# Kernel tuning notes

Measured on AMD Instinct MI355X. Metric: run time of the kernel, lower is better.

Reference implementation:

```python
import jax, jax.numpy as jnp
import numpy as np

B, S, IN, E, H, NH = 32, 1024, 16, 128, 256, 4
DH = E // NH
EPS = 1e-5


def _ln(x, g, b):
    mu = jnp.mean(x, axis=-1, keepdims=True)
    var = jnp.mean(jnp.square(x - mu), axis=-1, keepdims=True)
    return (x - mu) * jax.lax.rsqrt(var + EPS) * g + b


def setup_inputs() -> dict:
    key = jax.random.key(0)
    ks = iter(jax.random.split(key, 32))
    n = lambda shape, s=0.02: jax.random.normal(next(ks), shape, jnp.float32) * s
    inp = {
        "x": jax.random.normal(next(ks), (B, S, IN), jnp.float32),
        "mask": jax.random.uniform(next(ks), (B, S), jnp.float32),
        "embed_w": n((E, IN)), "embed_b": jnp.zeros((E,), jnp.float32),
        # 3 encoder layers, params stacked on leading layer axis
        "in_proj_w": n((3, 3 * E, E)), "in_proj_b": jnp.zeros((3, 3 * E), jnp.float32),
        "out_w": n((3, E, E)), "out_b": jnp.zeros((3, E), jnp.float32),
        "ln1_g": jnp.ones((3, E), jnp.float32), "ln1_b": jnp.zeros((3, E), jnp.float32),
        "ln2_g": jnp.ones((3, E), jnp.float32), "ln2_b": jnp.zeros((3, E), jnp.float32),
        "ffn_w1": n((3, E, E)), "ffn_b1": jnp.zeros((3, E), jnp.float32),
        "ffn_w2": n((3, E, E)), "ffn_b2": jnp.zeros((3, E), jnp.float32),
        "cls_w1": n((H, E)), "cls_b1": jnp.zeros((H,), jnp.float32),
        "cls_w2": n((H, H)), "cls_b2": jnp.zeros((H,), jnp.float32),
        "cls_w3": n((H, H)), "cls_b3": jnp.zeros((H,), jnp.float32),
        "cls_w4": n((1, H)), "cls_b4": jnp.zeros((1,), jnp.float32),
    }
    return inp


def _encoder_layer(x, ipw, ipb, ow, ob, g1, b1, g2, b2, w1, fb1, w2, fb2):
    # PyTorch TransformerEncoderLayer, norm_first=False (post-norm), relu FFN
    qkv = x @ ipw.T + ipb                      # [B,S,3E]
    q, k, v = jnp.split(qkv, 3, axis=-1)
    q = q.reshape(B, S, NH, DH).transpose(0, 2, 1, 3)
    k = k.reshape(B, S, NH, DH).transpose(0, 2, 1, 3)
    v = v.reshape(B, S, NH, DH).transpose(0, 2, 1, 3)
    scores = jnp.einsum("bhqd,bhkd->bhqk", q, k) / np.sqrt(DH)  # naive O(S^2) math SDPA
    attn = jax.nn.softmax(scores, axis=-1)
    o = jnp.einsum("bhqk,bhkd->bhqd", attn, v)
    o = o.transpose(0, 2, 1, 3).reshape(B, S, E) @ ow.T + ob
    x = _ln(x + o, g1, b1)
    ff = jax.nn.relu(x @ w1.T + fb1) @ w2.T + fb2
    return _ln(x + ff, g2, b2)


def reference(x, mask, embed_w, embed_b, in_proj_w, in_proj_b, out_w, out_b,
              ln1_g, ln1_b, ln2_g, ln2_b, ffn_w1, ffn_b1, ffn_w2, ffn_b2,
              cls_w1, cls_b1, cls_w2, cls_b2, cls_w3, cls_b3, cls_w4, cls_b4):
    h = jax.nn.relu(x @ embed_w.T + embed_b)   # [B,S,E]
    for i in range(3):
        h = _encoder_layer(h, in_proj_w[i], in_proj_b[i], out_w[i], out_b[i],
                           ln1_g[i], ln1_b[i], ln2_g[i], ln2_b[i],
                           ffn_w1[i], ffn_b1[i], ffn_w2[i], ffn_b2[i])
    pooled = jnp.sum(h * mask[:, :, None], axis=1)  # [B,E] masked sum pool
    z = jax.nn.relu(pooled @ cls_w1.T + cls_b1)
    z = jax.nn.relu(z @ cls_w2.T + cls_b2)
    z = jax.nn.relu(z @ cls_w3.T + cls_b3)
    return jax.nn.sigmoid(z @ cls_w4.T + cls_b4)    # [B,1]
```

## Files before the change

kernel.cpp:

```cpp
#include <hip/hip_runtime.h>
#include <hip/hip_bf16.h>
#include <math.h>

#define B 32
#define S 1024
#define IN_DIM 16
#define E 128
#define NH 4
#define DH 32
#define HDIM 256
#define ROWS (B*S)
#define EPS 1e-5f

#define N_IPW (3*384*128)
#define N_SQ  (3*128*128)
#define NCVT ((N_IPW + 3*N_SQ) / 256)

typedef __bf16 bf16x8 __attribute__((ext_vector_type(8)));
typedef __bf16 bf16x4 __attribute__((ext_vector_type(4)));
typedef __bf16 bf16x2 __attribute__((ext_vector_type(2)));
typedef float f32x4 __attribute__((ext_vector_type(4)));

#define MFMA16 __builtin_amdgcn_mfma_f32_16x16x32_bf16

union BF2U { bf16x2 b; unsigned int u; };
__device__ inline unsigned int pk2(float a, float b) {
    BF2U x; x.b[0] = (__bf16)a; x.b[1] = (__bf16)b; return x.u;
}

union U8 { bf16x8 v8; bf16x4 v4[2]; };
__device__ inline void st8(__bf16* p, bf16x8 v) {
    U8 u; u.v8 = v;
    *(bf16x4*)p = u.v4[0];
    *(bf16x4*)(p + 4) = u.v4[1];
}
__device__ inline bf16x8 ld8(const __bf16* p) {
    U8 u;
    u.v4[0] = *(const bf16x4*)p;
    u.v4[1] = *(const bf16x4*)(p + 4);
    return u.v8;
}

__global__ __launch_bounds__(256) void k_embedcvt(
        const float* __restrict__ ipw, const float* __restrict__ ow,
        const float* __restrict__ w1, const float* __restrict__ w2,
        __bf16* __restrict__ wbo,
        const float* __restrict__ x, const float* __restrict__ W,
        const float* __restrict__ bias, __bf16* __restrict__ hb)
{
    int t = threadIdx.x;
    if (blockIdx.x < NCVT) {
        int i = blockIdx.x * 256 + t;
        float v;
        if (i < N_IPW) v = ipw[i];
        else if (i < N_IPW + N_SQ) v = ow[i - N_IPW];
        else if (i < N_IPW + 2 * N_SQ) v = w1[i - N_IPW - N_SQ];
        else v = w2[i - N_IPW - 2 * N_SQ];
        wbo[i] = (__bf16)v;
        return;
    }
    int row0 = (blockIdx.x - NCVT) * 16;
    __shared__ float xs[16][16];
    xs[t >> 4][t & 15] = x[(row0 + (t >> 4)) * IN_DIM + (t & 15)];
    __syncthreads();
    int sub = t >> 7, tc = t & 127;
    float w[16];
#pragma unroll
    for (int i = 0; i < 16; ++i) w[i] = W[tc * 16 + i];
    float bb = bias[tc];
#pragma unroll
    for (int rr = 0; rr < 8; ++rr) {
        int lr = sub * 8 + rr;
        float acc = bb;
#pragma unroll
        for (int i = 0; i < 16; ++i) acc += xs[lr][i] * w[i];
        hb[(size_t)(row0 + lr) * E + tc] = (__bf16)fmaxf(acc, 0.f);
    }
}

__global__ __launch_bounds__(512, 2) void k_qkvattn(
        const __bf16* __restrict__ hb, const __bf16* __restrict__ Wip,
        const float* __restrict__ bip, __bf16* __restrict__ O)
{
    __shared__ __attribute__((aligned(16))) __bf16 Ksh[1024][36];
    __shared__ __attribute__((aligned(16))) __bf16 Vsh[32][1036];
    __shared__ __attribute__((aligned(16))) __bf16 Pm[8][16][68];

    int t = threadIdx.x, lane = t & 63, wv = t >> 6;
    int l15 = lane & 15, quad = lane >> 4;
    int lb = ((blockIdx.x & 7) << 5) | (blockIdx.x >> 3);
    int half = lb & 1, bh = lb >> 1;
    int hh = bh & 3, b = bh >> 2;

    const __bf16* hpanel = hb + (size_t)b * S * E;

    const float qscale = 0.1767766952966369f * 1.4426950408889634f * 8388608.0f;
    const float C2 = 1065101558.0f;
    const f32x4 cinit = {C2, C2, C2, C2};
    const f32x4 z4 = {0.f, 0.f, 0.f, 0.f};

    bf16x8 bWk[2][4], bWv[2][4];
#pragma unroll
    for (int df = 0; df < 2; ++df)
#pragma unroll
        for (int kc = 0; kc < 4; ++kc) {
            bWk[df][kc] = *(const bf16x8*)&Wip[(size_t)(128 + hh*32 + df*16 + l15)*128 + kc*32 + quad*8];
            bWv[df][kc] = *(const bf16x8*)&Wip[(size_t)(256 + hh*32 + df*16 + l15)*128 + kc*32 + quad*8];
        }
    float bk0 = bip[128 + hh*32 + l15],      bk1 = bip[128 + hh*32 + 16 + l15];
    float bvb0 = bip[256 + hh*32 + l15],     bvb1 = bip[256 + hh*32 + 16 + l15];

    int qrow0 = half*512 + wv*64;
    bf16x8 bQ[4];
    {
        bf16x8 bWq[2][4];
#pragma unroll
        for (int df = 0; df < 2; ++df)
#pragma unroll
            for (int kc = 0; kc < 4; ++kc)
                bWq[df][kc] = *(const bf16x8*)&Wip[(size_t)(hh*32 + df*16 + l15)*128 + kc*32 + quad*8];
        float bq0 = bip[hh*32 + l15], bq1 = bip[hh*32 + 16 + l15];
#pragma unroll
        for (int qf = 0; qf < 4; ++qf) {
            bf16x8 af[4];
#pragma unroll
            for (int kc = 0; kc < 4; ++kc)
                af[kc] = *(const bf16x8*)&hpanel[(size_t)(qrow0 + qf*16 + l15)*128 + kc*32 + quad*8];
            f32x4 a0 = z4, a1 = z4;
#pragma unroll
            for (int kc = 0; kc < 4; ++kc) {
                a0 = MFMA16(af[kc], bWq[0][kc], a0, 0, 0, 0);
                a1 = MFMA16(af[kc], bWq[1][kc], a1, 0, 0, 0);
            }
#pragma unroll
            for (int r = 0; r < 4; ++r) {
                Pm[wv][quad*4 + r][l15]      = (__bf16)((a0[r] + bq0) * qscale);
                Pm[wv][quad*4 + r][16 + l15] = (__bf16)((a1[r] + bq1) * qscale);
            }
            __asm__ __volatile__("" ::: "memory");
            bQ[qf] = ld8(&Pm[wv][l15][quad*8]);
            __asm__ __volatile__("" ::: "memory");
        }
    }

    {
        int srow = wv*16 + l15;
        bf16x8 af[4], ag[4];
#pragma unroll
        for (int kc = 0; kc < 4; ++kc)
            af[kc] = *(const bf16x8*)&hpanel[(size_t)srow*128 + kc*32 + quad*8];
        for (int c = 0; c < 8; ++c) {
            if (c < 7) {
#pragma unroll
                for (int kc = 0; kc < 4; ++kc)
                    ag[kc] = *(const bf16x8*)&hpanel[(size_t)((c+1)*128 + srow)*128 + kc*32 + quad*8];
            }
            f32x4 k0 = z4, k1 = z4, v0 = z4, v1 = z4;
#pragma unroll
            for (int kc = 0; kc < 4; ++kc) {
                k0 = MFMA16(af[kc], bWk[0][kc], k0, 0, 0, 0);
                k1 = MFMA16(af[kc], bWk[1][kc], k1, 0, 0, 0);
                v0 = MFMA16(af[kc], bWv[0][kc], v0, 0, 0, 0);
                v1 = MFMA16(af[kc], bWv[1][kc], v1, 0, 0, 0);
            }
            int s0 = c*128 + wv*16 + quad*4;
#pragma unroll
            for (int r = 0; r < 4; ++r) {
                Ksh[s0 + r][l15]      = (__bf16)(k0[r] + bk0);
                Ksh[s0 + r][16 + l15] = (__bf16)(k1[r] + bk1);
            }
            uint2 u0, u1;
            u0.x = pk2(v0[0] + bvb0, v0[1] + bvb0);
            u0.y = pk2(v0[2] + bvb0, v0[3] + bvb0);
            u1.x = pk2(v1[0] + bvb1, v1[1] + bvb1);
            u1.y = pk2(v1[2] + bvb1, v1[3] + bvb1);
            *(uint2*)&Vsh[l15][s0] = u0;
            *(uint2*)&Vsh[16 + l15][s0] = u1;
#pragma unroll
            for (int kc = 0; kc < 4; ++kc) af[kc] = ag[kc];
        }
    }
    __syncthreads();

    bf16x8 vones;
#pragma unroll
    for (int j = 0; j < 8; ++j) vones[j] = (__bf16)1.0f;
    f32x4 o[4][2], ol[4];
#pragma unroll
    for (int qf = 0; qf < 4; ++qf) {
        ol[qf] = z4; o[qf][0] = z4; o[qf][1] = z4;
    }

    for (int c = 0; c < 16; ++c) {
        bf16x8 aK[4], bV[2][2];
#pragma unroll
        for (int ck = 0; ck < 4; ++ck)
            aK[ck] = ld8(&Ksh[c*64 + ck*16 + l15][quad*8]);
#pragma unroll
        for (int kc = 0; kc < 2; ++kc) {
            bV[kc][0] = ld8(&Vsh[l15][c*64 + kc*32 + quad*8]);
            bV[kc][1] = ld8(&Vsh[16 + l15][c*64 + kc*32 + quad*8]);
        }
#pragma unroll
        for (int qf = 0; qf < 4; ++qf) {
            f32x4 sf[4];
#pragma unroll
            for (int ck = 0; ck < 4; ++ck)
                sf[ck] = MFMA16(aK[ck], bQ[qf], cinit, 0, 0, 0);
#pragma unroll
            for (int ck = 0; ck < 4; ++ck) {
                int i0 = (int)sf[ck][0];
                int i1 = (int)sf[ck][1];
                int i2 = (int)sf[ck][2];
                int i3 = (int)sf[ck][3];
                uint2 u;
                u.x = __builtin_amdgcn_perm((unsigned)i1, (unsigned)i0, 0x07060302u);
                u.y = __builtin_amdgcn_perm((unsigned)i3, (unsigned)i2, 0x07060302u);
                *(uint2*)&Pm[wv][l15][ck*16 + quad*4] = u;
            }
            __asm__ __volatile__("" ::: "memory");
#pragma unroll
            for (int kc = 0; kc < 2; ++kc) {
                bf16x8 ap = ld8(&Pm[wv][l15][kc*32 + quad*8]);
                o[qf][0] = MFMA16(ap, bV[kc][0], o[qf][0], 0, 0, 0);
                o[qf][1] = MFMA16(ap, bV[kc][1], o[qf][1], 0, 0, 0);
                ol[qf]   = MFMA16(ap, vones, ol[qf], 0, 0, 0);
            }
            __asm__ __volatile__("" ::: "memory");
        }
    }

#pragma unroll
    for (int qf = 0; qf < 4; ++qf)
#pragma unroll
        for (int r = 0; r < 4; ++r) {
            float linv = 1.f / ol[qf][r];
            int row = half*512 + wv*64 + qf*16 + quad*4 + r;
            __bf16* op = O + ((size_t)(b * S) + row) * E + hh*32;
            op[l15]      = (__bf16)(o[qf][0][r] * linv);
            op[16 + l15] = (__bf16)(o[qf][1][r] * linv);
        }
}

__global__ __launch_bounds__(256) void k_layer2(const __bf16* __restrict__ t0b,
        const __bf16* __restrict__ Wo, const float* __restrict__ ob,
        const float* __restrict__ g1, const float* __restrict__ bt1,
        const __bf16* __restrict__ W1, const float* __restrict__ b1v,
        const __bf16* __restrict__ W2, const float* __restrict__ b2v,
        const float* __restrict__ g2, const float* __restrict__ bt2,
        __bf16* __restrict__ hb)
{
    __shared__ __attribute__((aligned(16))) __bf16 As[64][132];
    __shared__ __attribute__((aligned(16))) __bf16 Ws[128][132];
    __shared__ float red[2][64][2];
    int t = threadIdx.x;
    int m0 = blockIdx.x * 64;
    int arow = t >> 2, acol = (t & 3) * 32;
    int wrow = t >> 1, wcol = (t & 1) * 64;
    {
        const __bf16* Ap = t0b + (size_t)(m0 + arow) * 128 + acol;
#pragma unroll
        for (int j = 0; j < 4; ++j)
            st8(&As[arow][acol + j * 8], *(const bf16x8*)&Ap[j * 8]);
        const __bf16* Wp = Wo + (size_t)wrow * 128 + wcol;
#pragma unroll
        for (int j = 0; j < 8; ++j)
            st8(&Ws[wrow][wcol + j * 8], *(const bf16x8*)&Wp[j * 8]);
    }
    __syncthreads();
    int lane = t & 63, wv = t >> 6;
    int l15 = lane & 15, quad = lane >> 4;
    int nh = wv & 1, mh = wv >> 1;
    f32x4 acc[4][2];

#pragma unroll
    for (int i = 0; i < 4; ++i)
#pragma unroll
        for (int j = 0; j < 2; ++j) acc[i][j] = (f32x4){0.f, 0.f, 0.f, 0.f};
#pragma unroll
    for (int kc = 0; kc < 4; ++kc) {
        bf16x8 aw[4], ba[2];
#pragma unroll
        for (int nc = 0; nc < 4; ++nc)
            aw[nc] = ld8(&Ws[nh * 64 + nc * 16 + l15][kc * 32 + quad * 8]);
#pragma unroll
        for (int mc = 0; mc < 2; ++mc)
            ba[mc] = ld8(&As[mh * 32 + mc * 16 + l15][kc * 32 + quad * 8]);
#pragma unroll
        for (int nc = 0; nc < 4; ++nc)
#pragma unroll
            for (int mc = 0; mc < 2; ++mc)
                acc[nc][mc] = MFMA16(aw[nc], ba[mc], acc[nc][mc], 0, 0, 0);
    }
    float s1[2] = {0.f, 0.f}, s2[2] = {0.f, 0.f};
#pragma unroll
    for (int nc = 0; nc < 4; ++nc) {
        float4 bv = *(const float4*)&ob[nh * 64 + nc * 16 + quad * 4];
#pragma unroll
        for (int mc = 0; mc < 2; ++mc) {
            int m = m0 + mh * 32 + mc * 16 + l15;
            bf16x4 rv = *(const bf16x4*)&hb[(size_t)m * 128 + nh * 64 + nc * 16 + quad * 4];
            acc[nc][mc][0] += bv.x + (float)rv[0];
            acc[nc][mc][1] += bv.y + (float)rv[1];
            acc[nc][mc][2] += bv.z + (float)rv[2];
            acc[nc][mc][3] += bv.w + (float)rv[3];
#pragma unroll
            for (int i = 0; i < 4; ++i) {
                s1[mc] += acc[nc][mc][i];
                s2[mc] += acc[nc][mc][i] * acc[nc][mc][i];
            }
        }
    }
#pragma unroll
    for (int mc = 0; mc < 2; ++mc) {
        s1[mc] += __shfl_xor(s1[mc], 16); s1[mc] += __shfl_xor(s1[mc], 32);
        s2[mc] += __shfl_xor(s2[mc], 16); s2[mc] += __shfl_xor(s2[mc], 32);
    }
    if (quad == 0) {
#pragma unroll
        for (int mc = 0; mc < 2; ++mc) {
            red[nh][mh * 32 + mc * 16 + l15][0] = s1[mc];
            red[nh][mh * 32 + mc * 16 + l15][1] = s2[mc];
        }
    }
    __syncthreads();
    float mu[2], rs[2];
#pragma unroll
    for (int mc = 0; mc < 2; ++mc) {
        int r = mh * 32 + mc * 16 + l15;
        float S1 = red[0][r][0] + red[1][r][0];
        float S2 = red[0][r][1] + red[1][r][1];
        mu[mc] = S1 * (1.f / 128.f);
        float var = S2 * (1.f / 128.f) - mu[mc] * mu[mc];
        rs[mc] = rsqrtf(var + EPS);
    }
    bf16x4 res2[4][2];
#pragma unroll
    for (int nc = 0; nc < 4; ++nc) {
        float4 gv = *(const float4*)&g1[nh * 64 + nc * 16 + quad * 4];
        float4 bb = *(const float4*)&bt1[nh * 64 + nc * 16 + quad * 4];
#pragma unroll
        for (int mc = 0; mc < 2; ++mc) {
            float o0 = (acc[nc][mc][0] - mu[mc]) * rs[mc] * gv.x + bb.x;
            float o1 = (acc[nc][mc][1] - mu[mc]) * rs[mc] * gv.y + bb.y;
            float o2 = (acc[nc][mc][2] - mu[mc]) * rs[mc] * gv.z + bb.z;
            float o3 = (acc[nc][mc][3] - mu[mc]) * rs[mc] * gv.w + bb.w;
            bf16x4 xb;
            xb[0] = (__bf16)o0; xb[1] = (__bf16)o1;
            xb[2] = (__bf16)o2; xb[3] = (__bf16)o3;
            res2[nc][mc] = xb;
            *(bf16x4*)&As[mh * 32 + mc * 16 + l15][nh * 64 + nc * 16 + quad * 4] = xb;
        }
    }
    {
        const __bf16* Wp = W1 + (size_t)wrow * 128 + wcol;
#pragma unroll
        for (int j = 0; j < 8; ++j)
            st8(&Ws[wrow][wcol + j * 8], *(const bf16x8*)&Wp[j * 8]);
    }
    __syncthreads();

#pragma unroll
    for (int i = 0; i < 4; ++i)
#pragma unroll
        for (int j = 0; j < 2; ++j) acc[i][j] = (f32x4){0.f, 0.f, 0.f, 0.f};
#pragma unroll
    for (int kc = 0; kc < 4; ++kc) {
        bf16x8 aw[4], ba[2];
#pragma unroll
        for (int nc = 0; nc < 4; ++nc)
            aw[nc] = ld8(&Ws[nh * 64 + nc * 16 + l15][kc * 32 + quad * 8]);
#pragma unroll
        for (int mc = 0; mc < 2; ++mc)
            ba[mc] = ld8(&As[mh * 32 + mc * 16 + l15][kc * 32 + quad * 8]);
#pragma unroll
        for (int nc = 0; nc < 4; ++nc)
#pragma unroll
            for (int mc = 0; mc < 2; ++mc)
                acc[nc][mc] = MFMA16(aw[nc], ba[mc], acc[nc][mc], 0, 0, 0);
    }
    __syncthreads();
#pragma unroll
    for (int nc = 0; nc < 4; ++nc) {
        float4 bv = *(const float4*)&b1v[nh * 64 + nc * 16 + quad * 4];
#pragma unroll
        for (int mc = 0; mc < 2; ++mc) {
            float v0 = fmaxf(acc[nc][mc][0] + bv.x, 0.f);
            float v1 = fmaxf(acc[nc][mc][1] + bv.y, 0.f);
            float v2 = fmaxf(acc[nc][mc][2] + bv.z, 0.f);
            float v3 = fmaxf(acc[nc][mc][3] + bv.w, 0.f);
            uint2 u; u.x = pk2(v0, v1); u.y = pk2(v2, v3);
            *(uint2*)&As[mh * 32 + mc * 16 + l15][nh * 64 + nc * 16 + quad * 4] = u;
        }
    }
    {
        const __bf16* Wp = W2 + (size_t)wrow * 128 + wcol;
#pragma unroll
        for (int j = 0; j < 8; ++j)
            st8(&Ws[wrow][wcol + j * 8], *(const bf16x8*)&Wp[j * 8]);
    }
    __syncthreads();

#pragma unroll
    for (int i = 0; i < 4; ++i)
#pragma unroll
        for (int j = 0; j < 2; ++j) acc[i][j] = (f32x4){0.f, 0.f, 0.f, 0.f};
#pragma unroll
    for (int kc = 0; kc < 4; ++kc) {
        bf16x8 aw[4], ba[2];
#pragma unroll
        for (int nc = 0; nc < 4; ++nc)
            aw[nc] = ld8(&Ws[nh * 64 + nc * 16 + l15][kc * 32 + quad * 8]);
#pragma unroll
        for (int mc = 0; mc < 2; ++mc)
            ba[mc] = ld8(&As[mh * 32 + mc * 16 + l15][kc * 32 + quad * 8]);
#pragma unroll
        for (int nc = 0; nc < 4; ++nc)
#pragma unroll
            for (int mc = 0; mc < 2; ++mc)
                acc[nc][mc] = MFMA16(aw[nc], ba[mc], acc[nc][mc], 0, 0, 0);
    }
    s1[0] = s1[1] = s2[0] = s2[1] = 0.f;
#pragma unroll
    for (int nc = 0; nc < 4; ++nc) {
        float4 bv = *(const float4*)&b2v[nh * 64 + nc * 16 + quad * 4];
#pragma unroll
        for (int mc = 0; mc < 2; ++mc) {
            acc[nc][mc][0] += bv.x + (float)res2[nc][mc][0];
            acc[nc][mc][1] += bv.y + (float)res2[nc][mc][1];
            acc[nc][mc][2] += bv.z + (float)res2[nc][mc][2];
            acc[nc][mc][3] += bv.w + (float)res2[nc][mc][3];
#pragma unroll
            for (int i = 0; i < 4; ++i) {
                s1[mc] += acc[nc][mc][i];
                s2[mc] += acc[nc][mc][i] * acc[nc][mc][i];
            }
        }
    }
#pragma unroll
    for (int mc = 0; mc < 2; ++mc) {
        s1[mc] += __shfl_xor(s1[mc], 16); s1[mc] += __shfl_xor(s1[mc], 32);
        s2[mc] += __shfl_xor(s2[mc], 16); s2[mc] += __shfl_xor(s2[mc], 32);
    }
    if (quad == 0) {
#pragma unroll
        for (int mc = 0; mc < 2; ++mc) {
            red[nh][mh * 32 + mc * 16 + l15][0] = s1[mc];
            red[nh][mh * 32 + mc * 16 + l15][1] = s2[mc];
        }
    }
    __syncthreads();
#pragma unroll
    for (int mc = 0; mc < 2; ++mc) {
        int r = mh * 32 + mc * 16 + l15;
        float S1 = red[0][r][0] + red[1][r][0];
        float S2 = red[0][r][1] + red[1][r][1];
        mu[mc] = S1 * (1.f / 128.f);
        float var = S2 * (1.f / 128.f) - mu[mc] * mu[mc];
        rs[mc] = rsqrtf(var + EPS);
    }
#pragma unroll
    for (int nc = 0; nc < 4; ++nc) {
        float4 gv = *(const float4*)&g2[nh * 64 + nc * 16 + quad * 4];
        float4 bb = *(const float4*)&bt2[nh * 64 + nc * 16 + quad * 4];
#pragma unroll
        for (int mc = 0; mc < 2; ++mc) {
            int m = m0 + mh * 32 + mc * 16 + l15;
            float o0 = (acc[nc][mc][0] - mu[mc]) * rs[mc] * gv.x + bb.x;
            float o1 = (acc[nc][mc][1] - mu[mc]) * rs[mc] * gv.y + bb.y;
            float o2 = (acc[nc][mc][2] - mu[mc]) * rs[mc] * gv.z + bb.z;
            float o3 = (acc[nc][mc][3] - mu[mc]) * rs[mc] * gv.w + bb.w;
            uint2 u; u.x = pk2(o0, o1); u.y = pk2(o2, o3);
            *(uint2*)&hb[(size_t)m * 128 + nh * 64 + nc * 16 + quad * 4] = u;
        }
    }
}

__global__ __launch_bounds__(128) void k_pool1(const __bf16* __restrict__ h,
        const float* __restrict__ mask, float* __restrict__ part)
{
    int bx = blockIdx.x;
    int b = bx >> 3, ch = bx & 7, t = threadIdx.x;
    float acc = 0.f;
    const __bf16* hp = h + (size_t)(b * S + ch * 128) * E + t;
    const float* mp = mask + b * S + ch * 128;
    for (int s = 0; s < 128; ++s) acc += (float)hp[(size_t)s * E] * mp[s];
    part[(size_t)bx * E + t] = acc;
}

__global__ __launch_bounds__(256) void k_head(const float* __restrict__ part,
        const float* __restrict__ cw1, const float* __restrict__ cb1,
        const float* __restrict__ cw2, const float* __restrict__ cb2,
        const float* __restrict__ cw3, const float* __restrict__ cb3,
        const float* __restrict__ cw4, const float* __restrict__ cb4,
        float* __restrict__ out)
{
    int b = blockIdx.x, t = threadIdx.x;
    __shared__ float p[128], za[256], zb[256];
    __shared__ float red4[4];
    if (t < 128) {
        float a = 0.f;
#pragma unroll
        for (int c = 0; c < 8; ++c) a += part[(size_t)(b * 8 + c) * 128 + t];
        p[t] = a;
    }
    __syncthreads();
    float a1 = cb1[t];
    for (int k = 0; k < 128; ++k) a1 += p[k] * cw1[t * 128 + k];
    za[t] = fmaxf(a1, 0.f);
    __syncthreads();
    float a2 = cb2[t];
    for (int k = 0; k < 256; ++k) a2 += za[k] * cw2[t * 256 + k];
    zb[t] = fmaxf(a2, 0.f);
    __syncthreads();
    float a3 = cb3[t];
    for (int k = 0; k < 256; ++k) a3 += zb[k] * cw3[t * 256 + k];
    float z3 = fmaxf(a3, 0.f);
    float prt = z3 * cw4[t];
#pragma unroll
    for (int o2 = 32; o2; o2 >>= 1) prt += __shfl_xor(prt, o2);
    if ((t & 63) == 0) red4[t >> 6] = prt;
    __syncthreads();
    if (t == 0) {
        float sum = red4[0] + red4[1] + red4[2] + red4[3] + cb4[0];
        out[b] = 1.f / (1.f + __expf(-sum));
    }
}

extern "C" void kernel_launch(void* const* d_in, const int* in_sizes, int n_in,
                              void* d_out, int out_size, void* d_ws, size_t ws_size,
                              hipStream_t stream)
{
    const float* x     = (const float*)d_in[0];
    const float* mask  = (const float*)d_in[1];
    const float* emb_w = (const float*)d_in[2];
    const float* emb_b = (const float*)d_in[3];
    const float* ipw   = (const float*)d_in[4];
    const float* ipb   = (const float*)d_in[5];
    const float* ow    = (const float*)d_in[6];
    const float* ob    = (const float*)d_in[7];
    const float* ln1g  = (const float*)d_in[8];
    const float* ln1b  = (const float*)d_in[9];
    const float* ln2g  = (const float*)d_in[10];
    const float* ln2b  = (const float*)d_in[11];
    const float* w1    = (const float*)d_in[12];
    const float* fb1   = (const float*)d_in[13];
    const float* w2    = (const float*)d_in[14];
    const float* fb2   = (const float*)d_in[15];
    const float* cw1   = (const float*)d_in[16];
    const float* cb1   = (const float*)d_in[17];
    const float* cw2   = (const float*)d_in[18];
    const float* cb2   = (const float*)d_in[19];
    const float* cw3   = (const float*)d_in[20];
    const float* cb3   = (const float*)d_in[21];
    const float* cw4   = (const float*)d_in[22];
    const float* cb4   = (const float*)d_in[23];

    char* p = (char*)d_ws;
    __bf16* hb   = (__bf16*)p;   p += (size_t)ROWS * E * 2;
    p += (size_t)ROWS * 256 * 2;
    p += (size_t)ROWS * 32 * 4 * 2 / 4;
    __bf16* t0b  = (__bf16*)p;   p += (size_t)ROWS * E * 2;
    __bf16* wb   = (__bf16*)p;   p += (size_t)(N_IPW + 3 * N_SQ) * 2;
    float* part  = (float*)p;    p += (size_t)B * 8 * E * 4;

    __bf16* wb_ipw = wb;
    __bf16* wb_ow  = wb + N_IPW;
    __bf16* wb_w1  = wb_ow + N_SQ;
    __bf16* wb_w2  = wb_w1 + N_SQ;

    k_embedcvt<<<NCVT + ROWS / 16, 256, 0, stream>>>(
        ipw, ow, w1, w2, wb, x, emb_w, emb_b, hb);
    for (int L = 0; L < 3; ++L) {
        k_qkvattn<<<B * NH * 2, 512, 0, stream>>>(
            hb, wb_ipw + (size_t)L * 384 * 128, ipb + L * 384, t0b);
        k_layer2<<<ROWS / 64, 256, 0, stream>>>(
            t0b, wb_ow + (size_t)L * 128 * 128, ob + L * 128,
            ln1g + L * E, ln1b + L * E,
            wb_w1 + (size_t)L * 128 * 128, fb1 + L * 128,
            wb_w2 + (size_t)L * 128 * 128, fb2 + L * 128,
            ln2g + L * E, ln2b + L * E, hb);
    }
    k_pool1<<<B * 8, 128, 0, stream>>>(hb, mask, part);
    k_head<<<B, 256, 0, stream>>>(part, cw1, cb1, cw2, cb2, cw3, cb3, cw4, cb4,
                                  (float*)d_out);
}
```

Before: 309.9 us.

## Double threads per block in attention and layer2 kernels, halving per-wave work

```diff
diff --git a/kernel.cpp b/kernel.cpp
--- a/kernel.cpp
+++ b/kernel.cpp
@@ -78,13 +78,13 @@
     }
 }
 
-__global__ __launch_bounds__(512, 2) void k_qkvattn(
+__global__ __launch_bounds__(1024, 4) void k_qkvattn(
         const __bf16* __restrict__ hb, const __bf16* __restrict__ Wip,
         const float* __restrict__ bip, __bf16* __restrict__ O)
 {
     __shared__ __attribute__((aligned(16))) __bf16 Ksh[1024][36];
     __shared__ __attribute__((aligned(16))) __bf16 Vsh[32][1036];
-    __shared__ __attribute__((aligned(16))) __bf16 Pm[8][16][68];
+    __shared__ __attribute__((aligned(16))) __bf16 Pm[16][16][36];
 
     int t = threadIdx.x, lane = t & 63, wv = t >> 6;
     int l15 = lane & 15, quad = lane >> 4;
@@ -99,19 +99,8 @@
     const f32x4 cinit = {C2, C2, C2, C2};
     const f32x4 z4 = {0.f, 0.f, 0.f, 0.f};
 
-    bf16x8 bWk[2][4], bWv[2][4];
-#pragma unroll
-    for (int df = 0; df < 2; ++df)
-#pragma unroll
-        for (int kc = 0; kc < 4; ++kc) {
-            bWk[df][kc] = *(const bf16x8*)&Wip[(size_t)(128 + hh*32 + df*16 + l15)*128 + kc*32 + quad*8];
-            bWv[df][kc] = *(const bf16x8*)&Wip[(size_t)(256 + hh*32 + df*16 + l15)*128 + kc*32 + quad*8];
-        }
-    float bk0 = bip[128 + hh*32 + l15],      bk1 = bip[128 + hh*32 + 16 + l15];
-    float bvb0 = bip[256 + hh*32 + l15],     bvb1 = bip[256 + hh*32 + 16 + l15];
-
-    int qrow0 = half*512 + wv*64;
-    bf16x8 bQ[4];
+    int qrow0 = half * 512 + wv * 32;
+    bf16x8 bQ[2];
     {
         bf16x8 bWq[2][4];
 #pragma unroll
@@ -121,7 +110,7 @@
                 bWq[df][kc] = *(const bf16x8*)&Wip[(size_t)(hh*32 + df*16 + l15)*128 + kc*32 + quad*8];
         float bq0 = bip[hh*32 + l15], bq1 = bip[hh*32 + 16 + l15];
 #pragma unroll
-        for (int qf = 0; qf < 4; ++qf) {
+        for (int qf = 0; qf < 2; ++qf) {
             bf16x8 af[4];
 #pragma unroll
             for (int kc = 0; kc < 4; ++kc)
@@ -144,17 +133,23 @@
     }
 
     {
-        int srow = wv*16 + l15;
-        bf16x8 af[4], ag[4];
-#pragma unroll
-        for (int kc = 0; kc < 4; ++kc)
-            af[kc] = *(const bf16x8*)&hpanel[(size_t)srow*128 + kc*32 + quad*8];
-        for (int c = 0; c < 8; ++c) {
-            if (c < 7) {
-#pragma unroll
-                for (int kc = 0; kc < 4; ++kc)
-                    ag[kc] = *(const bf16x8*)&hpanel[(size_t)((c+1)*128 + srow)*128 + kc*32 + quad*8];
-            }
+        bf16x8 bWk[2][4], bWv[2][4];
+#pragma unroll
+        for (int df = 0; df < 2; ++df)
+#pragma unroll
+            for (int kc = 0; kc < 4; ++kc) {
+                bWk[df][kc] = *(const bf16x8*)&Wip[(size_t)(128 + hh*32 + df*16 + l15)*128 + kc*32 + quad*8];
+                bWv[df][kc] = *(const bf16x8*)&Wip[(size_t)(256 + hh*32 + df*16 + l15)*128 + kc*32 + quad*8];
+            }
+        float bk0 = bip[128 + hh*32 + l15],  bk1 = bip[128 + hh*32 + 16 + l15];
+        float bvb0 = bip[256 + hh*32 + l15], bvb1 = bip[256 + hh*32 + 16 + l15];
+#pragma unroll
+        for (int c = 0; c < 4; ++c) {
+            int srow = c*256 + wv*16 + l15;
+            bf16x8 af[4];
+#pragma unroll
+            for (int kc = 0; kc < 4; ++kc)
+                af[kc] = *(const bf16x8*)&hpanel[(size_t)srow*128 + kc*32 + quad*8];
             f32x4 k0 = z4, k1 = z4, v0 = z4, v1 = z4;
 #pragma unroll
             for (int kc = 0; kc < 4; ++kc) {
@@ -163,7 +158,7 @@
                 v0 = MFMA16(af[kc], bWv[0][kc], v0, 0, 0, 0);
                 v1 = MFMA16(af[kc], bWv[1][kc], v1, 0, 0, 0);
             }
-            int s0 = c*128 + wv*16 + quad*4;
+            int s0 = c*256 + wv*16 + quad*4;
 #pragma unroll
             for (int r = 0; r < 4; ++r) {
                 Ksh[s0 + r][l15]      = (__bf16)(k0[r] + bk0);
@@ -176,8 +171,6 @@
             u1.y = pk2(v1[2] + bvb1, v1[3] + bvb1);
             *(uint2*)&Vsh[l15][s0] = u0;
             *(uint2*)&Vsh[16 + l15][s0] = u1;
-#pragma unroll
-            for (int kc = 0; kc < 4; ++kc) af[kc] = ag[kc];
         }
     }
     __syncthreads();
@@ -185,9 +178,9 @@
     bf16x8 vones;
 #pragma unroll
     for (int j = 0; j < 8; ++j) vones[j] = (__bf16)1.0f;
-    f32x4 o[4][2], ol[4];
-#pragma unroll
-    for (int qf = 0; qf < 4; ++qf) {
+    f32x4 o[2][2], ol[2];
+#pragma unroll
+    for (int qf = 0; qf < 2; ++qf) {
         ol[qf] = z4; o[qf][0] = z4; o[qf][1] = z4;
     }
 
@@ -202,47 +195,57 @@
             bV[kc][1] = ld8(&Vsh[16 + l15][c*64 + kc*32 + quad*8]);
         }
 #pragma unroll
-        for (int qf = 0; qf < 4; ++qf) {
+        for (int qf = 0; qf < 2; ++qf) {
             f32x4 sf[4];
 #pragma unroll
             for (int ck = 0; ck < 4; ++ck)
                 sf[ck] = MFMA16(aK[ck], bQ[qf], cinit, 0, 0, 0);
+            uint2 u[4];
 #pragma unroll
             for (int ck = 0; ck < 4; ++ck) {
                 int i0 = (int)sf[ck][0];
                 int i1 = (int)sf[ck][1];
                 int i2 = (int)sf[ck][2];
                 int i3 = (int)sf[ck][3];
-                uint2 u;
-                u.x = __builtin_amdgcn_perm((unsigned)i1, (unsigned)i0, 0x07060302u);
-                u.y = __builtin_amdgcn_perm((unsigned)i3, (unsigned)i2, 0x07060302u);
-                *(uint2*)&Pm[wv][l15][ck*16 + quad*4] = u;
-            }
+                u[ck].x = __builtin_amdgcn_perm((unsigned)i1, (unsigned)i0, 0x07060302u);
+                u[ck].y = __builtin_amdgcn_perm((unsigned)i3, (unsigned)i2, 0x07060302u);
+            }
+            *(uint2*)&Pm[wv][l15][quad*4]      = u[0];
+            *(uint2*)&Pm[wv][l15][16 + quad*4] = u[1];
             __asm__ __volatile__("" ::: "memory");
-#pragma unroll
-            for (int kc = 0; kc < 2; ++kc) {
-                bf16x8 ap = ld8(&Pm[wv][l15][kc*32 + quad*8]);
-                o[qf][0] = MFMA16(ap, bV[kc][0], o[qf][0], 0, 0, 0);
-                o[qf][1] = MFMA16(ap, bV[kc][1], o[qf][1], 0, 0, 0);
+            {
+                bf16x8 ap = ld8(&Pm[wv][l15][quad*8]);
+                o[qf][0] = MFMA16(ap, bV[0][0], o[qf][0], 0, 0, 0);
+                o[qf][1] = MFMA16(ap, bV[0][1], o[qf][1], 0, 0, 0);
                 ol[qf]   = MFMA16(ap, vones, ol[qf], 0, 0, 0);
             }
             __asm__ __volatile__("" ::: "memory");
-        }
-    }
-
-#pragma unroll
-    for (int qf = 0; qf < 4; ++qf)
+            *(uint2*)&Pm[wv][l15][quad*4]      = u[2];
+            *(uint2*)&Pm[wv][l15][16 + quad*4] = u[3];
+            __asm__ __volatile__("" ::: "memory");
+            {
+                bf16x8 ap = ld8(&Pm[wv][l15][quad*8]);
+                o[qf][0] = MFMA16(ap, bV[1][0], o[qf][0], 0, 0, 0);
+                o[qf][1] = MFMA16(ap, bV[1][1], o[qf][1], 0, 0, 0);
+                ol[qf]   = MFMA16(ap, vones, ol[qf], 0, 0, 0);
+            }
+            __asm__ __volatile__("" ::: "memory");
+        }
+    }
+
+#pragma unroll
+    for (int qf = 0; qf < 2; ++qf)
 #pragma unroll
         for (int r = 0; r < 4; ++r) {
             float linv = 1.f / ol[qf][r];
-            int row = half*512 + wv*64 + qf*16 + quad*4 + r;
+            int row = half*512 + wv*32 + qf*16 + quad*4 + r;
             __bf16* op = O + ((size_t)(b * S) + row) * E + hh*32;
             op[l15]      = (__bf16)(o[qf][0][r] * linv);
             op[16 + l15] = (__bf16)(o[qf][1][r] * linv);
         }
 }
 
-__global__ __launch_bounds__(256) void k_layer2(const __bf16* __restrict__ t0b,
+__global__ __launch_bounds__(512, 4) void k_layer2(const __bf16* __restrict__ t0b,
         const __bf16* __restrict__ Wo, const float* __restrict__ ob,
         const float* __restrict__ g1, const float* __restrict__ bt1,
         const __bf16* __restrict__ W1, const float* __restrict__ b1v,
@@ -255,224 +258,176 @@
     __shared__ float red[2][64][2];
     int t = threadIdx.x;
     int m0 = blockIdx.x * 64;
-    int arow = t >> 2, acol = (t & 3) * 32;
-    int wrow = t >> 1, wcol = (t & 1) * 64;
+    int arow = t >> 3, acol = (t & 7) * 16;
+    int wrow = t >> 2, wcol = (t & 3) * 32;
     {
         const __bf16* Ap = t0b + (size_t)(m0 + arow) * 128 + acol;
 #pragma unroll
-        for (int j = 0; j < 4; ++j)
+        for (int j = 0; j < 2; ++j)
             st8(&As[arow][acol + j * 8], *(const bf16x8*)&Ap[j * 8]);
         const __bf16* Wp = Wo + (size_t)wrow * 128 + wcol;
 #pragma unroll
-        for (int j = 0; j < 8; ++j)
+        for (int j = 0; j < 4; ++j)
             st8(&Ws[wrow][wcol + j * 8], *(const bf16x8*)&Wp[j * 8]);
     }
     __syncthreads();
     int lane = t & 63, wv = t >> 6;
     int l15 = lane & 15, quad = lane >> 4;
     int nh = wv & 1, mh = wv >> 1;
-    f32x4 acc[4][2];
-
-#pragma unroll
-    for (int i = 0; i < 4; ++i)
-#pragma unroll
-        for (int j = 0; j < 2; ++j) acc[i][j] = (f32x4){0.f, 0.f, 0.f, 0.f};
+    f32x4 acc[4];
+
+#pragma unroll
+    for (int i = 0; i < 4; ++i) acc[i] = (f32x4){0.f, 0.f, 0.f, 0.f};
 #pragma unroll
     for (int kc = 0; kc < 4; ++kc) {
-        bf16x8 aw[4], ba[2];
+        bf16x8 aw[4], ba;
 #pragma unroll
         for (int nc = 0; nc < 4; ++nc)
             aw[nc] = ld8(&Ws[nh * 64 + nc * 16 + l15][kc * 32 + quad * 8]);
-#pragma unroll
-        for (int mc = 0; mc < 2; ++mc)
-            ba[mc] = ld8(&As[mh * 32 + mc * 16 + l15][kc * 32 + quad * 8]);
+        ba = ld8(&As[mh * 16 + l15][kc * 32 + quad * 8]);
 #pragma unroll
         for (int nc = 0; nc < 4; ++nc)
-#pragma unroll
-            for (int mc = 0; mc < 2; ++mc)
-                acc[nc][mc] = MFMA16(aw[nc], ba[mc], acc[nc][mc], 0, 0, 0);
-    }
-    float s1[2] = {0.f, 0.f}, s2[2] = {0.f, 0.f};
+            acc[nc] = MFMA16(aw[nc], ba, acc[nc], 0, 0, 0);
+    }
+    float s1 = 0.f, s2 = 0.f;
+    int m = m0 + mh * 16 + l15;
 #pragma unroll
     for (int nc = 0; nc < 4; ++nc) {
         float4 bv = *(const float4*)&ob[nh * 64 + nc * 16 + quad * 4];
-#pragma unroll
-        for (int mc = 0; mc < 2; ++mc) {
-            int m = m0 + mh * 32 + mc * 16 + l15;
-            bf16x4 rv = *(const bf16x4*)&hb[(size_t)m * 128 + nh * 64 + nc * 16 + quad * 4];
-            acc[nc][mc][0] += bv.x + (float)rv[0];
-            acc[nc][mc][1] += bv.y + (float)rv[1];
-            acc[nc][mc][2] += bv.z + (float)rv[2];
-            acc[nc][mc][3] += bv.w + (float)rv[3];
-#pragma unroll
-            for (int i = 0; i < 4; ++i) {
-                s1[mc] += acc[nc][mc][i];
-                s2[mc] += acc[nc][mc][i] * acc[nc][mc][i];
-            }
-        }
-    }
-#pragma unroll
-    for (int mc = 0; mc < 2; ++mc) {
-        s1[mc] += __shfl_xor(s1[mc], 16); s1[mc] += __shfl_xor(s1[mc], 32);
-        s2[mc] += __shfl_xor(s2[mc], 16); s2[mc] += __shfl_xor(s2[mc], 32);
-    }
+        bf16x4 rv = *(const bf16x4*)&hb[(size_t)m * 128 + nh * 64 + nc * 16 + quad * 4];
+        acc[nc][0] += bv.x + (float)rv[0];
+        acc[nc][1] += bv.y + (float)rv[1];
+        acc[nc][2] += bv.z + (float)rv[2];
+        acc[nc][3] += bv.w + (float)rv[3];
+#pragma unroll
+        for (int i = 0; i < 4; ++i) {
+            s1 += acc[nc][i];
+            s2 += acc[nc][i] * acc[nc][i];
+        }
+    }
+    s1 += __shfl_xor(s1, 16); s1 += __shfl_xor(s1, 32);
+    s2 += __shfl_xor(s2, 16); s2 += __shfl_xor(s2, 32);
     if (quad == 0) {
-#pragma unroll
-        for (int mc = 0; mc < 2; ++mc) {
-            red[nh][mh * 32 + mc * 16 + l15][0] = s1[mc];
-            red[nh][mh * 32 + mc * 16 + l15][1] = s2[mc];
-        }
-    }
-    __syncthreads();
-    float mu[2], rs[2];
-#pragma unroll
-    for (int mc = 0; mc < 2; ++mc) {
-        int r = mh * 32 + mc * 16 + l15;
+        red[nh][mh * 16 + l15][0] = s1;
+        red[nh][mh * 16 + l15][1] = s2;
+    }
+    __syncthreads();
+    float mu, rs;
+    {
+        int r = mh * 16 + l15;
         float S1 = red[0][r][0] + red[1][r][0];
         float S2 = red[0][r][1] + red[1][r][1];
-        mu[mc] = S1 * (1.f / 128.f);
-        float var = S2 * (1.f / 128.f) - mu[mc] * mu[mc];
-        rs[mc] = rsqrtf(var + EPS);
-    }
-    bf16x4 res2[4][2];
+        mu = S1 * (1.f / 128.f);
+        float var = S2 * (1.f / 128.f) - mu * mu;
+        rs = rsqrtf(var + EPS);
+    }
+    bf16x4 res2[4];
 #pragma unroll
     for (int nc = 0; nc < 4; ++nc) {
         float4 gv = *(const float4*)&g1[nh * 64 + nc * 16 + quad * 4];
         float4 bb = *(const float4*)&bt1[nh * 64 + nc * 16 + quad * 4];
-#pragma unroll
-        for (int mc = 0; mc < 2; ++mc) {
-            float o0 = (acc[nc][mc][0] - mu[mc]) * rs[mc] * gv.x + bb.x;
-            float o1 = (acc[nc][mc][1] - mu[mc]) * rs[mc] * gv.y + bb.y;
-            float o2 = (acc[nc][mc][2] - mu[mc]) * rs[mc] * gv.z + bb.z;
-            float o3 = (acc[nc][mc][3] - mu[mc]) * rs[mc] * gv.w + bb.w;
-            bf16x4 xb;
-            xb[0] = (__bf16)o0; xb[1] = (__bf16)o1;
-            xb[2] = (__bf16)o2; xb[3] = (__bf16)o3;
-            res2[nc][mc] = xb;
-            *(bf16x4*)&As[mh * 32 + mc * 16 + l15][nh * 64 + nc * 16 + quad * 4] = xb;
-        }
+        float o0 = (acc[nc][0] - mu) * rs * gv.x + bb.x;
+        float o1 = (acc[nc][1] - mu) * rs * gv.y + bb.y;
+        float o2 = (acc[nc][2] - mu) * rs * gv.z + bb.z;
+        float o3 = (acc[nc][3] - mu) * rs * gv.w + bb.w;
+        bf16x4 xb;
+        xb[0] = (__bf16)o0; xb[1] = (__bf16)o1;
+        xb[2] = (__bf16)o2; xb[3] = (__bf16)o3;
+        res2[nc] = xb;
+        *(bf16x4*)&As[mh * 16 + l15][nh * 64 + nc * 16 + quad * 4] = xb;
     }
     {
         const __bf16* Wp = W1 + (size_t)wrow * 128 + wcol;
 #pragma unroll
-        for (int j = 0; j < 8; ++j)
+        for (int j = 0; j < 4; ++j)
             st8(&Ws[wrow][wcol + j * 8], *(const bf16x8*)&Wp[j * 8]);
     }
     __syncthreads();
 
 #pragma unroll
-    for (int i = 0; i < 4; ++i)
-#pragma unroll
-        for (int j = 0; j < 2; ++j) acc[i][j] = (f32x4){0.f, 0.f, 0.f, 0.f};
+    for (int i = 0; i < 4; ++i) acc[i] = (f32x4){0.f, 0.f, 0.f, 0.f};
 #pragma unroll
     for (int kc = 0; kc < 4; ++kc) {
-        bf16x8 aw[4], ba[2];
+        bf16x8 aw[4], ba;
 #pragma unroll
         for (int nc = 0; nc < 4; ++nc)
             aw[nc] = ld8(&Ws[nh * 64 + nc * 16 + l15][kc * 32 + quad * 8]);
-#pragma unroll
-        for (int mc = 0; mc < 2; ++mc)
-            ba[mc] = ld8(&As[mh * 32 + mc * 16 + l15][kc * 32 + quad * 8]);
+        ba = ld8(&As[mh * 16 + l15][kc * 32 + quad * 8]);
 #pragma unroll
         for (int nc = 0; nc < 4; ++nc)
-#pragma unroll
-            for (int mc = 0; mc < 2; ++mc)
-                acc[nc][mc] = MFMA16(aw[nc], ba[mc], acc[nc][mc], 0, 0, 0);
+            acc[nc] = MFMA16(aw[nc], ba, acc[nc], 0, 0, 0);
     }
     __syncthreads();
 #pragma unroll
     for (int nc = 0; nc < 4; ++nc) {
         float4 bv = *(const float4*)&b1v[nh * 64 + nc * 16 + quad * 4];
-#pragma unroll
-        for (int mc = 0; mc < 2; ++mc) {
-            float v0 = fmaxf(acc[nc][mc][0] + bv.x, 0.f);
-            float v1 = fmaxf(acc[nc][mc][1] + bv.y, 0.f);
-            float v2 = fmaxf(acc[nc][mc][2] + bv.z, 0.f);
-            float v3 = fmaxf(acc[nc][mc][3] + bv.w, 0.f);
-            uint2 u; u.x = pk2(v0, v1); u.y = pk2(v2, v3);
-            *(uint2*)&As[mh * 32 + mc * 16 + l15][nh * 64 + nc * 16 + quad * 4] = u;
-        }
+        float v0 = fmaxf(acc[nc][0] + bv.x, 0.f);
+        float v1 = fmaxf(acc[nc][1] + bv.y, 0.f);
+        float v2 = fmaxf(acc[nc][2] + bv.z, 0.f);
+        float v3 = fmaxf(acc[nc][3] + bv.w, 0.f);
+        uint2 u; u.x = pk2(v0, v1); u.y = pk2(v2, v3);
+        *(uint2*)&As[mh * 16 + l15][nh * 64 + nc * 16 + quad * 4] = u;
     }
     {
         const __bf16* Wp = W2 + (size_t)wrow * 128 + wcol;
 #pragma unroll
-        for (int j = 0; j < 8; ++j)
+        for (int j = 0; j < 4; ++j)
             st8(&Ws[wrow][wcol + j * 8], *(const bf16x8*)&Wp[j * 8]);
     }
     __syncthreads();
 
 #pragma unroll
-    for (int i = 0; i < 4; ++i)
-#pragma unroll
-        for (int j = 0; j < 2; ++j) acc[i][j] = (f32x4){0.f, 0.f, 0.f, 0.f};
+    for (int i = 0; i < 4; ++i) acc[i] = (f32x4){0.f, 0.f, 0.f, 0.f};
 #pragma unroll
     for (int kc = 0; kc < 4; ++kc) {
-        bf16x8 aw[4], ba[2];
+        bf16x8 aw[4], ba;
 #pragma unroll
         for (int nc = 0; nc < 4; ++nc)
             aw[nc] = ld8(&Ws[nh * 64 + nc * 16 + l15][kc * 32 + quad * 8]);
-#pragma unroll
-        for (int mc = 0; mc < 2; ++mc)
-            ba[mc] = ld8(&As[mh * 32 + mc * 16 + l15][kc * 32 + quad * 8]);
+        ba = ld8(&As[mh * 16 + l15][kc * 32 + quad * 8]);
 #pragma unroll
         for (int nc = 0; nc < 4; ++nc)
-#pragma unroll
-            for (int mc = 0; mc < 2; ++mc)
-                acc[nc][mc] = MFMA16(aw[nc], ba[mc], acc[nc][mc], 0, 0, 0);
-    }
-    s1[0] = s1[1] = s2[0] = s2[1] = 0.f;
+            acc[nc] = MFMA16(aw[nc], ba, acc[nc], 0, 0, 0);
+    }
+    s1 = 0.f; s2 = 0.f;
 #pragma unroll
     for (int nc = 0; nc < 4; ++nc) {
         float4 bv = *(const float4*)&b2v[nh * 64 + nc * 16 + quad * 4];
-#pragma unroll
-        for (int mc = 0; mc < 2; ++mc) {
-            acc[nc][mc][0] += bv.x + (float)res2[nc][mc][0];
-            acc[nc][mc][1] += bv.y + (float)res2[nc][mc][1];
-            acc[nc][mc][2] += bv.z + (float)res2[nc][mc][2];
-            acc[nc][mc][3] += bv.w + (float)res2[nc][mc][3];
-#pragma unroll
-            for (int i = 0; i < 4; ++i) {
-                s1[mc] += acc[nc][mc][i];
-                s2[mc] += acc[nc][mc][i] * acc[nc][mc][i];
-            }
-        }
-    }
-#pragma unroll
-    for (int mc = 0; mc < 2; ++mc) {
-        s1[mc] += __shfl_xor(s1[mc], 16); s1[mc] += __shfl_xor(s1[mc], 32);
-        s2[mc] += __shfl_xor(s2[mc], 16); s2[mc] += __shfl_xor(s2[mc], 32);
-    }
+        acc[nc][0] += bv.x + (float)res2[nc][0];
+        acc[nc][1] += bv.y + (float)res2[nc][1];
+        acc[nc][2] += bv.z + (float)res2[nc][2];
+        acc[nc][3] += bv.w + (float)res2[nc][3];
+#pragma unroll
+        for (int i = 0; i < 4; ++i) {
+            s1 += acc[nc][i];
+            s2 += acc[nc][i] * acc[nc][i];
+        }
+    }
+    s1 += __shfl_xor(s1, 16); s1 += __shfl_xor(s1, 32);
+    s2 += __shfl_xor(s2, 16); s2 += __shfl_xor(s2, 32);
     if (quad == 0) {
-#pragma unroll
-        for (int mc = 0; mc < 2; ++mc) {
-            red[nh][mh * 32 + mc * 16 + l15][0] = s1[mc];
-            red[nh][mh * 32 + mc * 16 + l15][1] = s2[mc];
-        }
-    }
-    __syncthreads();
-#pragma unroll
-    for (int mc = 0; mc < 2; ++mc) {
-        int r = mh * 32 + mc * 16 + l15;
+        red[nh][mh * 16 + l15][0] = s1;
+        red[nh][mh * 16 + l15][1] = s2;
+    }
+    __syncthreads();
+    {
+        int r = mh * 16 + l15;
         float S1 = red[0][r][0] + red[1][r][0];
         float S2 = red[0][r][1] + red[1][r][1];
-        mu[mc] = S1 * (1.f / 128.f);
-        float var = S2 * (1.f / 128.f) - mu[mc] * mu[mc];
-        rs[mc] = rsqrtf(var + EPS);
+        mu = S1 * (1.f / 128.f);
+        float var = S2 * (1.f / 128.f) - mu * mu;
+        rs = rsqrtf(var + EPS);
     }
 #pragma unroll
     for (int nc = 0; nc < 4; ++nc) {
         float4 gv = *(const float4*)&g2[nh * 64 + nc * 16 + quad * 4];
         float4 bb = *(const float4*)&bt2[nh * 64 + nc * 16 + quad * 4];
-#pragma unroll
-        for (int mc = 0; mc < 2; ++mc) {
-            int m = m0 + mh * 32 + mc * 16 + l15;
-            float o0 = (acc[nc][mc][0] - mu[mc]) * rs[mc] * gv.x + bb.x;
-            float o1 = (acc[nc][mc][1] - mu[mc]) * rs[mc] * gv.y + bb.y;
-            float o2 = (acc[nc][mc][2] - mu[mc]) * rs[mc] * gv.z + bb.z;
-            float o3 = (acc[nc][mc][3] - mu[mc]) * rs[mc] * gv.w + bb.w;
-            uint2 u; u.x = pk2(o0, o1); u.y = pk2(o2, o3);
-            *(uint2*)&hb[(size_t)m * 128 + nh * 64 + nc * 16 + quad * 4] = u;
-        }
+        float o0 = (acc[nc][0] - mu) * rs * gv.x + bb.x;
+        float o1 = (acc[nc][1] - mu) * rs * gv.y + bb.y;
+        float o2 = (acc[nc][2] - mu) * rs * gv.z + bb.z;
+        float o3 = (acc[nc][3] - mu) * rs * gv.w + bb.w;
+        uint2 u; u.x = pk2(o0, o1); u.y = pk2(o2, o3);
+        *(uint2*)&hb[(size_t)m * 128 + nh * 64 + nc * 16 + quad * 4] = u;
     }
 }
 
@@ -572,9 +527,9 @@
     k_embedcvt<<<NCVT + ROWS / 16, 256, 0, stream>>>(
         ipw, ow, w1, w2, wb, x, emb_w, emb_b, hb);
     for (int L = 0; L < 3; ++L) {
-        k_qkvattn<<<B * NH * 2, 512, 0, stream>>>(
+        k_qkvattn<<<B * NH * 2, 1024, 0, stream>>>(
             hb, wb_ipw + (size_t)L * 384 * 128, ipb + L * 384, t0b);
-        k_layer2<<<ROWS / 64, 256, 0, stream>>>(
+        k_layer2<<<ROWS / 64, 512, 0, stream>>>(
             t0b, wb_ow + (size_t)L * 128 * 128, ob + L * 128,
             ln1g + L * E, ln1b + L * E,
             wb_w1 + (size_t)L * 128 * 128, fb1 + L * 128,
```

Measured after the change: 316.5 us. 2.1% more time.
